# Performance work log

Hardware: AMD Instinct MI355X
Metric: run time of the kernel (lower is better)

The kernel has to match this reference:

```python
import jax, jax.numpy as jnp
import numpy as np

NEG = -9e15
SLOPE = 0.02

def setup_inputs() -> dict:
    key = jax.random.key(0)
    k1, k2, k3, k4 = jax.random.split(key, 4)
    N, IN, OUT = 16384, 128, 64
    x = jax.random.normal(k1, (N, IN), dtype=jnp.float32)
    adj = jax.random.randint(k2, (N, N), 0, 2, dtype=jnp.int32)
    weight = jax.random.normal(k3, (IN, OUT), dtype=jnp.float32) * (1.0 / np.sqrt(IN))
    att_weight = jax.random.normal(k4, (2 * OUT, 1), dtype=jnp.float32) * (1.0 / np.sqrt(2 * OUT))
    return {"x": x, "adj": adj, "weight": weight, "att_weight": att_weight}

def reference(x, adj, weight, att_weight):
    out_feature = weight.shape[1]
    Wh = x @ weight                                   # [N, out]
    f_i = Wh @ att_weight[:out_feature, :]            # [N, 1] source term
    f_j = Wh @ att_weight[out_feature:, :]            # [N, 1] dest term
    e = f_i + f_j.T                                   # [N, N] additive scores
    e = jax.nn.leaky_relu(e, negative_slope=SLOPE)
    att = jnp.where(adj > 0, e, NEG)
    att = jax.nn.softmax(att, axis=1)                 # masked row softmax
    h_prime = att @ Wh                                # [N, out]
    return jax.nn.elu(h_prime)                        # concat=True -> elu
```

## Files before the change

kernel.cpp:

```cpp
#include <hip/hip_runtime.h>
#include <cstdint>
#include <cstddef>

#define GN   16384
#define GIN  128
#define GOUT 64
#define NCH  16
#define LOG2E 1.44269504088896340736f

typedef __attribute__((ext_vector_type(8))) short short8;
typedef __attribute__((ext_vector_type(4))) float f32x4;
typedef __attribute__((ext_vector_type(4))) int   int4v;

__device__ __forceinline__ unsigned short f2bf(float f) {
  unsigned u = __float_as_uint(f);
  return (unsigned short)((u + 0x8000u) >> 16);
}

__device__ __forceinline__ unsigned short f2bf_rne(float f) {
  unsigned u = __float_as_uint(f);
  u += 0x7FFFu + ((u >> 16) & 1u);
  return (unsigned short)(u >> 16);
}

__global__ __launch_bounds__(256) void mask_kernel(
    const int* __restrict__ adj, unsigned char* __restrict__ msk)
{
  const unsigned nb = (unsigned)((size_t)GN * (size_t)GN / 8);
  const unsigned stride = gridDim.x * 256;
  for (unsigned b = blockIdx.x * 256 + threadIdx.x; b < nb; b += stride) {
    const int4v* p = (const int4v*)(adj + (size_t)b * 8);
    int4v x0 = __builtin_nontemporal_load(p);
    int4v x1 = __builtin_nontemporal_load(p + 1);
    unsigned by = (unsigned)(x0.x != 0)
                | ((unsigned)(x0.y != 0) << 1)
                | ((unsigned)(x0.z != 0) << 2)
                | ((unsigned)(x0.w != 0) << 3)
                | ((unsigned)(x1.x != 0) << 4)
                | ((unsigned)(x1.y != 0) << 5)
                | ((unsigned)(x1.z != 0) << 6)
                | ((unsigned)(x1.w != 0) << 7);
    msk[b] = (unsigned char)by;
  }
}

__global__ __launch_bounds__(256) void prep_kernel(
    const float* __restrict__ x, const float* __restrict__ w,
    const float* __restrict__ aw, unsigned short* __restrict__ wpk,
    float* __restrict__ fs2, float* __restrict__ fd2)
{
  __shared__ float ws[GIN * GOUT];
  __shared__ float red[2][64][4];

  const int t = threadIdx.x;
  const int rb = blockIdx.x * 64;

  for (int i = t; i < (GIN * GOUT) / 4; i += 256)
    ((float4*)ws)[i] = ((const float4*)w)[i];
  __syncthreads();

  const int r = t & 63, s = t >> 6;
  const int row = rb + r;
  const float* xr = x + (size_t)row * GIN;

  float acc[16];
#pragma unroll
  for (int d = 0; d < 16; ++d) acc[d] = 0.f;

  for (int kk = 0; kk < GIN; kk += 4) {
    float4 xv = *(const float4*)(xr + kk);
    float xa[4] = {xv.x, xv.y, xv.z, xv.w};
#pragma unroll
    for (int u = 0; u < 4; ++u) {
#pragma unroll
      for (int d = 0; d < 16; ++d)
        acc[d] += xa[u] * ws[(kk + u) * GOUT + s * 16 + d];
    }
  }

  const int jc = row >> 5;
  const int qq = (row & 31) >> 3;
  const int tt = row & 7;
  float psrc = 0.f, pdst = 0.f;
#pragma unroll
  for (int d = 0; d < 16; ++d) {
    const int dg = s * 16 + d;
    psrc += acc[d] * aw[dg];
    pdst += acc[d] * aw[GOUT + dg];
    const int f = dg >> 4, n = dg & 15;
    wpk[(size_t)jc * 4096 + f * 1024 + (qq * 16 + n) * 8 + tt] = f2bf_rne(acc[d]);
  }
  red[0][r][s] = psrc;
  red[1][r][s] = pdst;
  __syncthreads();
  if (s == 0) {
    float a_ = red[0][r][0] + red[0][r][1] + red[0][r][2] + red[0][r][3];
    float b_ = red[1][r][0] + red[1][r][1] + red[1][r][2] + red[1][r][3];
    fs2[row] = a_ * LOG2E;
    fd2[row] = b_ * LOG2E;
  }
}

__global__ __launch_bounds__(256, 4) void gat_main(
    const unsigned* __restrict__ bmw, const unsigned short* __restrict__ wpk,
    const float* __restrict__ fs2, const float* __restrict__ fd2,
    float* __restrict__ nump, float* __restrict__ denp)
{
  const int wave  = blockIdx.x * 4 + (threadIdx.x >> 6);
  const int lane  = threadIdx.x & 63;
  const int strip = wave & 511;
  const int chunk = wave >> 9;
  const int m = lane & 15;
  const int q = lane >> 4;
  const int q8 = q << 3;

  int   row0 = strip * 32 + m;
  int   row1 = row0 + 16;
  float fs0 = fs2[row0];
  float fs1 = fs2[row1];
  const unsigned* __restrict__ bmr0 = bmw + (size_t)row0 * (GN / 32);
  const unsigned* __restrict__ bmr1 = bmw + (size_t)row1 * (GN / 32);

  const int CW = GN / NCH;
  const int j0 = chunk * CW;
  const float4* __restrict__ fdv  = (const float4*)fd2;
  const short8* __restrict__ wpk8 = (const short8*)wpk;

  f32x4 acc0[4], acc1[4];
  f32x4 accd0, accd1;
  accd0 = (f32x4){0.f, 0.f, 0.f, 0.f};
  accd1 = (f32x4){0.f, 0.f, 0.f, 0.f};
#pragma unroll
  for (int b = 0; b < 4; ++b) {
    acc0[b] = (f32x4){0.f, 0.f, 0.f, 0.f};
    acc1[b] = (f32x4){0.f, 0.f, 0.f, 0.f};
  }

  short8 b_ones;
#pragma unroll
  for (int i = 0; i < 8; ++i) b_ones[i] = (short)0x3F80;

  auto pelem = [&](unsigned byte, int t, float fd, float fsv) -> unsigned short {
    float sv = fsv + fd;
    float lv = fmaxf(sv, 0.02f * sv);
    float pe = __builtin_amdgcn_exp2f(lv);
    pe = (byte & (1u << t)) ? pe : 0.f;
    return f2bf(pe);
  };

  auto mk_af = [&](unsigned byte, float4 fA, float4 fB, float fsv) -> short8 {
    short8 af;
    af[0] = (short)pelem(byte, 0, fA.x, fsv);
    af[1] = (short)pelem(byte, 1, fA.y, fsv);
    af[2] = (short)pelem(byte, 2, fA.z, fsv);
    af[3] = (short)pelem(byte, 3, fA.w, fsv);
    af[4] = (short)pelem(byte, 4, fB.x, fsv);
    af[5] = (short)pelem(byte, 5, fB.y, fsv);
    af[6] = (short)pelem(byte, 6, fB.z, fsv);
    af[7] = (short)pelem(byte, 7, fB.w, fsv);
    return af;
  };

  auto LOADSTEP = [&](int j, unsigned& w0, unsigned& w1, float4& g0, float4& g1) {
    const int wi = j >> 5;
    const int i4 = (j >> 2) + (q << 1);
    w0 = bmr0[wi];
    w1 = bmr1[wi];
    g0 = fdv[i4];
    g1 = fdv[i4 + 1];
  };

  auto COMPS = [&](int j, unsigned w0, unsigned w1, float4 g0, float4 g1) {
    const int wi = j >> 5;
    const short8* wb = wpk8 + (size_t)wi * 512 + lane;
    short8 b0 = wb[0];
    short8 b1 = wb[128];
    short8 b2 = wb[256];
    short8 b3 = wb[384];

    {
      const unsigned byte = (w0 >> q8) & 0xffu;
      short8 af = mk_af(byte, g0, g1, fs0);
      acc0[0] = __builtin_amdgcn_mfma_f32_16x16x32_bf16(af, b0, acc0[0], 0, 0, 0);
      acc0[1] = __builtin_amdgcn_mfma_f32_16x16x32_bf16(af, b1, acc0[1], 0, 0, 0);
      acc0[2] = __builtin_amdgcn_mfma_f32_16x16x32_bf16(af, b2, acc0[2], 0, 0, 0);
      acc0[3] = __builtin_amdgcn_mfma_f32_16x16x32_bf16(af, b3, acc0[3], 0, 0, 0);
      accd0   = __builtin_amdgcn_mfma_f32_16x16x32_bf16(af, b_ones, accd0, 0, 0, 0);
    }
    {
      const unsigned byte = (w1 >> q8) & 0xffu;
      short8 af = mk_af(byte, g0, g1, fs1);
      acc1[0] = __builtin_amdgcn_mfma_f32_16x16x32_bf16(af, b0, acc1[0], 0, 0, 0);
      acc1[1] = __builtin_amdgcn_mfma_f32_16x16x32_bf16(af, b1, acc1[1], 0, 0, 0);
      acc1[2] = __builtin_amdgcn_mfma_f32_16x16x32_bf16(af, b2, acc1[2], 0, 0, 0);
      acc1[3] = __builtin_amdgcn_mfma_f32_16x16x32_bf16(af, b3, acc1[3], 0, 0, 0);
      accd1   = __builtin_amdgcn_mfma_f32_16x16x32_bf16(af, b_ones, accd1, 0, 0, 0);
    }
  };

  unsigned wA0, wA1, wB0, wB1;
  float4 fA0, fA1, fB0, fB1;

  LOADSTEP(j0, wA0, wA1, fA0, fA1);
#pragma unroll 1
  for (int j = j0; j < j0 + CW; j += 64) {
    LOADSTEP(j + 32, wB0, wB1, fB0, fB1);
    COMPS(j, wA0, wA1, fA0, fA1);
    int jn = j + 64;
    jn = (jn < j0 + CW) ? jn : j0;
    LOADSTEP(jn, wA0, wA1, fA0, fA1);
    COMPS(j + 32, wB0, wB1, fB0, fB1);
  }

  float* np = nump + (size_t)chunk * GN * GOUT;
  float* dp = denp + (size_t)chunk * GN;
  {
    const int orow0 = strip * 32 + q * 4;
#pragma unroll
    for (int r = 0; r < 4; ++r) {
      float* nr = np + (size_t)(orow0 + r) * GOUT + m;
      __builtin_nontemporal_store(acc0[0][r], nr + 0);
      __builtin_nontemporal_store(acc0[1][r], nr + 16);
      __builtin_nontemporal_store(acc0[2][r], nr + 32);
      __builtin_nontemporal_store(acc0[3][r], nr + 48);
      if (m == 0) dp[orow0 + r] = accd0[r];
    }
  }
  {
    const int orow0 = strip * 32 + 16 + q * 4;
#pragma unroll
    for (int r = 0; r < 4; ++r) {
      float* nr = np + (size_t)(orow0 + r) * GOUT + m;
      __builtin_nontemporal_store(acc1[0][r], nr + 0);
      __builtin_nontemporal_store(acc1[1][r], nr + 16);
      __builtin_nontemporal_store(acc1[2][r], nr + 32);
      __builtin_nontemporal_store(acc1[3][r], nr + 48);
      if (m == 0) dp[orow0 + r] = accd1[r];
    }
  }
}

__global__ __launch_bounds__(256) void fin_kernel(
    const float* __restrict__ nump, const float* __restrict__ denp,
    float* __restrict__ out)
{
  const int g = blockIdx.x * 256 + threadIdx.x;
  if (g >= GN * GOUT) return;
  const int row = g >> 6;
  float s = 0.f, d = 0.f;
#pragma unroll
  for (int c = 0; c < NCH; ++c) {
    s += nump[(size_t)c * GN * GOUT + g];
    d += denp[(size_t)c * GN + row];
  }
  float v = s / d;
  out[g] = (v > 0.f) ? v : expm1f(v);
}

extern "C" void kernel_launch(void* const* d_in, const int* in_sizes, int n_in,
                              void* d_out, int out_size, void* d_ws, size_t ws_size,
                              hipStream_t stream) {
  const float* x   = (const float*)d_in[0];
  const int*   adj = (const int*)d_in[1];
  const float* w   = (const float*)d_in[2];
  const float* aw  = (const float*)d_in[3];
  float* out = (float*)d_out;

  float* nump = (float*)d_ws;
  float* denp = nump + (size_t)NCH * GN * GOUT;
  float* fs2  = denp + (size_t)NCH * GN;
  float* fd2  = fs2 + GN;
  unsigned short* wpk = (unsigned short*)(fd2 + GN);
  unsigned char* msk = (unsigned char*)(wpk + (size_t)512 * 4096);

  mask_kernel<<<2048, 256, 0, stream>>>(adj, msk);
  prep_kernel<<<GN / 64, 256, 0, stream>>>(x, w, aw, wpk, fs2, fd2);
  gat_main<<<(GN / 32) * NCH / 4, 256, 0, stream>>>((const unsigned*)msk, wpk, fs2, fd2, nump, denp);
  fin_kernel<<<(GN * GOUT) / 256, 256, 0, stream>>>(nump, denp, out);
}
```

Before: 1.489 ms.

## Fuse adjacency bitmask packing into main GAT kernel via shared memory

```diff
diff --git a/kernel.cpp b/kernel.cpp
--- a/kernel.cpp
+++ b/kernel.cpp
@@ -5,7 +5,7 @@
 #define GN   16384
 #define GIN  128
 #define GOUT 64
-#define NCH  16
+#define NCH  8
 #define LOG2E 1.44269504088896340736f
 
 typedef __attribute__((ext_vector_type(8))) short short8;
@@ -21,27 +21,6 @@
   unsigned u = __float_as_uint(f);
   u += 0x7FFFu + ((u >> 16) & 1u);
   return (unsigned short)(u >> 16);
-}
-
-__global__ __launch_bounds__(256) void mask_kernel(
-    const int* __restrict__ adj, unsigned char* __restrict__ msk)
-{
-  const unsigned nb = (unsigned)((size_t)GN * (size_t)GN / 8);
-  const unsigned stride = gridDim.x * 256;
-  for (unsigned b = blockIdx.x * 256 + threadIdx.x; b < nb; b += stride) {
-    const int4v* p = (const int4v*)(adj + (size_t)b * 8);
-    int4v x0 = __builtin_nontemporal_load(p);
-    int4v x1 = __builtin_nontemporal_load(p + 1);
-    unsigned by = (unsigned)(x0.x != 0)
-                | ((unsigned)(x0.y != 0) << 1)
-                | ((unsigned)(x0.z != 0) << 2)
-                | ((unsigned)(x0.w != 0) << 3)
-                | ((unsigned)(x1.x != 0) << 4)
-                | ((unsigned)(x1.y != 0) << 5)
-                | ((unsigned)(x1.z != 0) << 6)
-                | ((unsigned)(x1.w != 0) << 7);
-    msk[b] = (unsigned char)by;
-  }
 }
 
 __global__ __launch_bounds__(256) void prep_kernel(
@@ -101,35 +80,56 @@
   }
 }
 
-__global__ __launch_bounds__(256, 4) void gat_main(
-    const unsigned* __restrict__ bmw, const unsigned short* __restrict__ wpk,
+__global__ __launch_bounds__(256, 2) void gat_main(
+    const int* __restrict__ adj, const unsigned short* __restrict__ wpk,
     const float* __restrict__ fs2, const float* __restrict__ fd2,
     float* __restrict__ nump, float* __restrict__ denp)
 {
-  const int wave  = blockIdx.x * 4 + (threadIdx.x >> 6);
-  const int lane  = threadIdx.x & 63;
-  const int strip = wave & 511;
-  const int chunk = wave >> 9;
+  __shared__ unsigned mk[4][32][66];
+
+  const int w    = threadIdx.x >> 6;
+  const int lane = threadIdx.x & 63;
+  const int br    = blockIdx.x & 127;
+  const int chunk = blockIdx.x >> 7;
+  const int strip32 = br * 4 + w;
   const int m = lane & 15;
   const int q = lane >> 4;
   const int q8 = q << 3;
 
-  int   row0 = strip * 32 + m;
-  int   row1 = row0 + 16;
-  float fs0 = fs2[row0];
-  float fs1 = fs2[row1];
-  const unsigned* __restrict__ bmr0 = bmw + (size_t)row0 * (GN / 32);
-  const unsigned* __restrict__ bmr1 = bmw + (size_t)row1 * (GN / 32);
-
   const int CW = GN / NCH;
   const int j0 = chunk * CW;
+
+  {
+    const int4v* ap = (const int4v*)(adj + (size_t)(strip32 * 32) * GN + j0);
+    const int lane8 = lane * 8;
+#pragma unroll 1
+    for (int r = 0; r < 32; ++r) {
+      unsigned bits = 0;
+#pragma unroll
+      for (int k = 0; k < 8; ++k) {
+        int4v v = ap[lane8 + k];
+        bits |= ((unsigned)(v.x != 0) << (k * 4))
+              | ((unsigned)(v.y != 0) << (k * 4 + 1))
+              | ((unsigned)(v.z != 0) << (k * 4 + 2))
+              | ((unsigned)(v.w != 0) << (k * 4 + 3));
+      }
+      mk[w][r][lane] = bits;
+      ap += GN / 4;
+    }
+  }
+  __syncthreads();
+
+  const int row0 = strip32 * 32 + m;
+  const int row1 = row0 + 16;
+  const float fs0 = fs2[row0];
+  const float fs1 = fs2[row1];
+
   const float4* __restrict__ fdv  = (const float4*)fd2;
   const short8* __restrict__ wpk8 = (const short8*)wpk;
 
   f32x4 acc0[4], acc1[4];
   f32x4 accd0, accd1;
-  accd0 = (f32x4){0.f, 0.f, 0.f, 0.f};
-  accd1 = (f32x4){0.f, 0.f, 0.f, 0.f};
+  accd0 = accd1 = (f32x4){0.f, 0.f, 0.f, 0.f};
 #pragma unroll
   for (int b = 0; b < 4; ++b) {
     acc0[b] = (f32x4){0.f, 0.f, 0.f, 0.f};
@@ -161,26 +161,25 @@
     return af;
   };
 
-  auto LOADSTEP = [&](int j, unsigned& w0, unsigned& w1, float4& g0, float4& g1) {
-    const int wi = j >> 5;
+#pragma unroll 1
+  for (int j = j0; j < j0 + CW; j += 32) {
     const int i4 = (j >> 2) + (q << 1);
-    w0 = bmr0[wi];
-    w1 = bmr1[wi];
-    g0 = fdv[i4];
-    g1 = fdv[i4 + 1];
-  };
-
-  auto COMPS = [&](int j, unsigned w0, unsigned w1, float4 g0, float4 g1) {
-    const int wi = j >> 5;
-    const short8* wb = wpk8 + (size_t)wi * 512 + lane;
-    short8 b0 = wb[0];
-    short8 b1 = wb[128];
-    short8 b2 = wb[256];
-    short8 b3 = wb[384];
+    const int wi = (j - j0) >> 5;
+
+    const unsigned w0 = mk[w][m][wi];
+    const unsigned w1 = mk[w][m + 16][wi];
+    const float4 f0 = fdv[i4];
+    const float4 f1 = fdv[i4 + 1];
+
+    const short8* wb = wpk8 + (size_t)(j >> 5) * 512 + lane;
+    const short8 b0 = wb[0];
+    const short8 b1 = wb[128];
+    const short8 b2 = wb[256];
+    const short8 b3 = wb[384];
 
     {
       const unsigned byte = (w0 >> q8) & 0xffu;
-      short8 af = mk_af(byte, g0, g1, fs0);
+      short8 af = mk_af(byte, f0, f1, fs0);
       acc0[0] = __builtin_amdgcn_mfma_f32_16x16x32_bf16(af, b0, acc0[0], 0, 0, 0);
       acc0[1] = __builtin_amdgcn_mfma_f32_16x16x32_bf16(af, b1, acc0[1], 0, 0, 0);
       acc0[2] = __builtin_amdgcn_mfma_f32_16x16x32_bf16(af, b2, acc0[2], 0, 0, 0);
@@ -189,33 +188,19 @@
     }
     {
       const unsigned byte = (w1 >> q8) & 0xffu;
-      short8 af = mk_af(byte, g0, g1, fs1);
+      short8 af = mk_af(byte, f0, f1, fs1);
       acc1[0] = __builtin_amdgcn_mfma_f32_16x16x32_bf16(af, b0, acc1[0], 0, 0, 0);
       acc1[1] = __builtin_amdgcn_mfma_f32_16x16x32_bf16(af, b1, acc1[1], 0, 0, 0);
       acc1[2] = __builtin_amdgcn_mfma_f32_16x16x32_bf16(af, b2, acc1[2], 0, 0, 0);
       acc1[3] = __builtin_amdgcn_mfma_f32_16x16x32_bf16(af, b3, acc1[3], 0, 0, 0);
       accd1   = __builtin_amdgcn_mfma_f32_16x16x32_bf16(af, b_ones, accd1, 0, 0, 0);
     }
-  };
-
-  unsigned wA0, wA1, wB0, wB1;
-  float4 fA0, fA1, fB0, fB1;
-
-  LOADSTEP(j0, wA0, wA1, fA0, fA1);
-#pragma unroll 1
-  for (int j = j0; j < j0 + CW; j += 64) {
-    LOADSTEP(j + 32, wB0, wB1, fB0, fB1);
-    COMPS(j, wA0, wA1, fA0, fA1);
-    int jn = j + 64;
-    jn = (jn < j0 + CW) ? jn : j0;
-    LOADSTEP(jn, wA0, wA1, fA0, fA1);
-    COMPS(j + 32, wB0, wB1, fB0, fB1);
   }
 
   float* np = nump + (size_t)chunk * GN * GOUT;
   float* dp = denp + (size_t)chunk * GN;
   {
-    const int orow0 = strip * 32 + q * 4;
+    const int orow0 = strip32 * 32 + q * 4;
 #pragma unroll
     for (int r = 0; r < 4; ++r) {
       float* nr = np + (size_t)(orow0 + r) * GOUT + m;
@@ -227,7 +212,7 @@
     }
   }
   {
-    const int orow0 = strip * 32 + 16 + q * 4;
+    const int orow0 = strip32 * 32 + 16 + q * 4;
 #pragma unroll
     for (int r = 0; r < 4; ++r) {
       float* nr = np + (size_t)(orow0 + r) * GOUT + m;
@@ -271,10 +256,8 @@
   float* fs2  = denp + (size_t)NCH * GN;
   float* fd2  = fs2 + GN;
   unsigned short* wpk = (unsigned short*)(fd2 + GN);
-  unsigned char* msk = (unsigned char*)(wpk + (size_t)512 * 4096);
-
-  mask_kernel<<<2048, 256, 0, stream>>>(adj, msk);
+
   prep_kernel<<<GN / 64, 256, 0, stream>>>(x, w, aw, wpk, fs2, fd2);
-  gat_main<<<(GN / 32) * NCH / 4, 256, 0, stream>>>((const unsigned*)msk, wpk, fs2, fd2, nump, denp);
+  gat_main<<<(GN / 128) * NCH, 256, 0, stream>>>(adj, wpk, fs2, fd2, nump, denp);
   fin_kernel<<<(GN * GOUT) / 256, 256, 0, stream>>>(nump, denp, out);
 }
```

New measurement: 1.398 ms. -6.1%, faster.
